# Optimization experiments

Measured on AMD Instinct MI355X. Metric: run time of the kernel, lower is better.

The kernel has to match this reference:

```python
import jax, jax.numpy as jnp
import numpy as np

N, D = 16384, 2048


def setup_inputs() -> dict:
    key = jax.random.key(0)
    k1, k2 = jax.random.split(key)
    x = jax.random.normal(k1, (N, D), dtype=jnp.float32)
    mask = jax.random.randint(k2, (N, D), 0, 2) > 0
    return {"x": x, "mask": mask}


def _masked_sparsemax(z, m):
    """Project each row of z onto the simplex restricted to positions where m is True.

    Fully batched equivalent of the TF per-row map_fn/cond/boolean_mask version.
    z: [..., D] float, m: [..., D] bool. Returns p with p>=0, sum over active = 1
    (all-zeros row if no active entries).
    """
    d = z.shape[-1]
    num_active = jnp.sum(m, axis=-1, keepdims=True)                 # [..., 1] int
    # Masked entries sort to the tail (-inf), so the first num_active sorted
    # entries are exactly the active values in descending order.
    z_neg = jnp.where(m, z, -jnp.inf)
    z_sorted = -jnp.sort(-z_neg, axis=-1)                           # descending
    k_int = jnp.arange(1, d + 1)
    k = k_int.astype(z.dtype)
    active_pos = k_int <= num_active                                # [..., D]
    # cumsum over active sorted entries only (zeros beyond num_active)
    csum = jnp.cumsum(jnp.where(active_pos, z_sorted, 0.0), axis=-1)
    # support condition: z_(k) - (csum_k - 1)/k > 0  <=>  k*z_(k) > csum_k - 1
    cond = (z_sorted * k > (csum - 1.0)) & active_pos
    rho = jnp.sum(cond, axis=-1, keepdims=True)                     # support size
    rho_idx = jnp.clip(rho - 1, 0, d - 1)
    csum_rho = jnp.take_along_axis(csum, rho_idx, axis=-1)
    theta = (csum_rho - 1.0) / jnp.maximum(rho, 1).astype(z.dtype)
    p_valid = jnp.maximum(z - theta, 0.0)
    # TF invalid_branch fallback: uniform over active entries (unreachable in
    # exact arithmetic since k=1 always satisfies cond, kept for faithfulness)
    p_uniform = 1.0 / jnp.maximum(num_active, 1).astype(z.dtype)
    p = jnp.where(rho > 0, p_valid, p_uniform)
    return jnp.where(m & (num_active > 0), p, 0.0)


def reference(x, mask):
    # axis = -1: project along the last axis (the TF layer transposes the
    # chosen axis to last; with axis=-1 that transpose is the identity).
    return _masked_sparsemax(x, mask)
```

## Files before the change

kernel.cpp:

```cpp
#include <hip/hip_runtime.h>
#include <math.h>


constexpr int D    = 2048;
constexpr int WPB  = 4;
constexpr int TPB  = WPB * 64;
constexpr int EPT  = D / 64;
constexpr int CHK  = EPT / 4;

__global__ __launch_bounds__(TPB) void sparsemax_kernel(
    const float* __restrict__ x,
    const int*   __restrict__ mask,
    float*       __restrict__ out,
    int n_rows)
{
    const int wave = threadIdx.x >> 6;
    const int lane = threadIdx.x & 63;
    const int row  = blockIdx.x * WPB + wave;
    if (row >= n_rows) return;

    const size_t rbase = (size_t)row * D;

    float z[EPT];
    #pragma unroll
    for (int c = 0; c < CHK; ++c) {
        const size_t off = rbase + (size_t)(c * 256 + lane * 4);
        const float4 a = *(const float4*)(x    + off);
        const int4   m = *(const int4*)  (mask + off);
        z[c * 4 + 0] = m.x ? a.x : -INFINITY;
        z[c * 4 + 1] = m.y ? a.y : -INFINITY;
        z[c * 4 + 2] = m.z ? a.z : -INFINITY;
        z[c * 4 + 3] = m.w ? a.w : -INFINITY;
    }

    float theta = -INFINITY;
    float prevC = -1.0f;

    for (int it = 0; it < 128; ++it) {
        float ps = 0.0f, pc = 0.0f;
        #pragma unroll
        for (int k = 0; k < EPT; ++k) {
            if (z[k] > theta) { ps += z[k]; pc += 1.0f; }
        }
        #pragma unroll
        for (int off = 32; off > 0; off >>= 1) {
            ps += __shfl_xor(ps, off, 64);
            pc += __shfl_xor(pc, off, 64);
        }
        if (pc == 0.0f) { theta = INFINITY; break; }
        if (pc == prevC) break;
        theta = (ps - 1.0f) / pc;
        prevC = pc;
    }

    #pragma unroll
    for (int c = 0; c < CHK; ++c) {
        const size_t off = rbase + (size_t)(c * 256 + lane * 4);
        float4 o;
        o.x = fmaxf(z[c * 4 + 0] - theta, 0.0f);
        o.y = fmaxf(z[c * 4 + 1] - theta, 0.0f);
        o.z = fmaxf(z[c * 4 + 2] - theta, 0.0f);
        o.w = fmaxf(z[c * 4 + 3] - theta, 0.0f);
        *(float4*)(out + off) = o;
    }
}

extern "C" void kernel_launch(void* const* d_in, const int* in_sizes, int n_in,
                              void* d_out, int out_size, void* d_ws, size_t ws_size,
                              hipStream_t stream) {
    const float* x    = (const float*)d_in[0];
    const int*   mask = (const int*)  d_in[1];
    float*       out  = (float*)d_out;
    const int n_rows = in_sizes[0] / D;
    const int blocks = (n_rows + WPB - 1) / WPB;
    sparsemax_kernel<<<blocks, TPB, 0, stream>>>(x, mask, out, n_rows);
}
```

Baseline: 313.6 us.

## Start sparsemax threshold search at max-1 and use ballot-based support counting

The threshold iteration now starts from the row maximum minus one instead of negative infinity. It updates theta with a Newton-style step based on the sum of positive excesses. The support count comes from wave ballots plus popcount instead of a per-lane float counter and shuffle reduction. The intent is fewer iterations and cheaper reductions per iteration, at the cost of an extra max reduction and one ballot per element per iteration.

Result: no change. 310.8 us (-0.9%).

```diff
diff --git a/kernel.cpp b/kernel.cpp
--- a/kernel.cpp
+++ b/kernel.cpp
@@ -33,24 +33,48 @@
         z[c * 4 + 3] = m.w ? a.w : -INFINITY;
     }
 
-    float theta = -INFINITY;
-    float prevC = -1.0f;
+    float m0 = z[0], m1 = z[1], m2 = z[2], m3 = z[3];
+    #pragma unroll
+    for (int k = 4; k < EPT; k += 4) {
+        m0 = fmaxf(m0, z[k + 0]);
+        m1 = fmaxf(m1, z[k + 1]);
+        m2 = fmaxf(m2, z[k + 2]);
+        m3 = fmaxf(m3, z[k + 3]);
+    }
+    float gmax = fmaxf(fmaxf(m0, m1), fmaxf(m2, m3));
+    #pragma unroll
+    for (int off = 32; off > 0; off >>= 1)
+        gmax = fmaxf(gmax, __shfl_xor(gmax, off, 64));
 
-    for (int it = 0; it < 128; ++it) {
-        float ps = 0.0f, pc = 0.0f;
-        #pragma unroll
-        for (int k = 0; k < EPT; ++k) {
-            if (z[k] > theta) { ps += z[k]; pc += 1.0f; }
+    float theta;
+    if (gmax == -INFINITY) {
+        theta = INFINITY;
+    } else {
+        theta = gmax - 1.0f;
+        int prevC = -1;
+        for (int it = 0; it < 64; ++it) {
+            float f0 = 0.0f, f1 = 0.0f, f2 = 0.0f, f3 = 0.0f;
+            #pragma unroll
+            for (int k = 0; k < EPT; k += 4) {
+                f0 += fmaxf(z[k + 0] - theta, 0.0f);
+                f1 += fmaxf(z[k + 1] - theta, 0.0f);
+                f2 += fmaxf(z[k + 2] - theta, 0.0f);
+                f3 += fmaxf(z[k + 3] - theta, 0.0f);
+            }
+            float f = (f0 + f1) + (f2 + f3);
+            int C = 0;
+            #pragma unroll
+            for (int k = 0; k < EPT; ++k)
+                C += (int)__popcll(__ballot(z[k] > theta));
+            #pragma unroll
+            for (int off = 32; off > 0; off >>= 1)
+                f += __shfl_xor(f, off, 64);
+
+            if (C == 0) break;
+            if (C == prevC) break;
+            theta += (f - 1.0f) / (float)C;
+            prevC = C;
         }
-        #pragma unroll
-        for (int off = 32; off > 0; off >>= 1) {
-            ps += __shfl_xor(ps, off, 64);
-            pc += __shfl_xor(pc, off, 64);
-        }
-        if (pc == 0.0f) { theta = INFINITY; break; }
-        if (pc == prevC) break;
-        theta = (ps - 1.0f) / pc;
-        prevC = pc;
     }
 
     #pragma unroll
```

## Process two rows per wave with max-initialized Newton threshold iteration

Applied to the files above, without the earlier changes.

Each wave now handles two rows, interleaving their loads and threshold iterations to raise memory-level parallelism. The threshold search starts at max-1 and takes Newton-style steps on the sum of clipped values, with the support count taken from ballot/popcount instead of per-lane float counts. Output uses nontemporal stores, and launch bounds request higher occupancy. The cost is doubled register pressure (two 32-element rows per lane), which under the occupancy hint may cause spills, and a changed convergence path that could shift floating-point results slightly.

Measured after the change: 328.9 us. 1.05x slower.

```diff
diff --git a/kernel.cpp b/kernel.cpp
--- a/kernel.cpp
+++ b/kernel.cpp
@@ -2,13 +2,15 @@
 #include <math.h>
 
 
-constexpr int D    = 2048;
-constexpr int WPB  = 4;
-constexpr int TPB  = WPB * 64;
-constexpr int EPT  = D / 64;
-constexpr int CHK  = EPT / 4;
+constexpr int D   = 2048;
+constexpr int TPB = 256;
+constexpr int EPT = D / 64;
+constexpr int CHK = EPT / 4;
+constexpr int RPB = 2 * (TPB / 64);
 
-__global__ __launch_bounds__(TPB) void sparsemax_kernel(
+typedef float nt_f4 __attribute__((ext_vector_type(4)));
+
+__global__ __launch_bounds__(TPB, 4) void sparsemax_kernel(
     const float* __restrict__ x,
     const int*   __restrict__ mask,
     float*       __restrict__ out,
@@ -16,52 +18,144 @@
 {
     const int wave = threadIdx.x >> 6;
     const int lane = threadIdx.x & 63;
-    const int row  = blockIdx.x * WPB + wave;
-    if (row >= n_rows) return;
+    const int g    = blockIdx.x * (TPB / 64) + wave;
+    const int rA   = g * 2;
+    const int rB   = rA + 1;
+    if (rA >= n_rows) return;
+    const bool hasB = (rB < n_rows);
 
-    const size_t rbase = (size_t)row * D;
+    const size_t baseA = (size_t)rA * D;
+    const size_t baseB = (size_t)rB * D;
 
-    float z[EPT];
+    float4 xa[CHK]; int4 ma[CHK];
     #pragma unroll
     for (int c = 0; c < CHK; ++c) {
-        const size_t off = rbase + (size_t)(c * 256 + lane * 4);
-        const float4 a = *(const float4*)(x    + off);
-        const int4   m = *(const int4*)  (mask + off);
-        z[c * 4 + 0] = m.x ? a.x : -INFINITY;
-        z[c * 4 + 1] = m.y ? a.y : -INFINITY;
-        z[c * 4 + 2] = m.z ? a.z : -INFINITY;
-        z[c * 4 + 3] = m.w ? a.w : -INFINITY;
+        const size_t off = baseA + (size_t)(c * 256 + lane * 4);
+        xa[c] = *(const float4*)(x    + off);
+        ma[c] = *(const int4*)  (mask + off);
+    }
+    float zA[EPT];
+    #pragma unroll
+    for (int c = 0; c < CHK; ++c) {
+        zA[c * 4 + 0] = ma[c].x ? xa[c].x : -INFINITY;
+        zA[c * 4 + 1] = ma[c].y ? xa[c].y : -INFINITY;
+        zA[c * 4 + 2] = ma[c].z ? xa[c].z : -INFINITY;
+        zA[c * 4 + 3] = ma[c].w ? xa[c].w : -INFINITY;
     }
 
-    float theta = -INFINITY;
-    float prevC = -1.0f;
+    float4 xb[CHK]; int4 mb[CHK];
+    if (hasB) {
+        #pragma unroll
+        for (int c = 0; c < CHK; ++c) {
+            const size_t off = baseB + (size_t)(c * 256 + lane * 4);
+            xb[c] = *(const float4*)(x    + off);
+            mb[c] = *(const int4*)  (mask + off);
+        }
+    }
 
-    for (int it = 0; it < 128; ++it) {
-        float ps = 0.0f, pc = 0.0f;
+    float m0 = zA[0], m1 = zA[1], m2 = zA[2], m3 = zA[3];
+    #pragma unroll
+    for (int k = 4; k < EPT; k += 4) {
+        m0 = fmaxf(m0, zA[k + 0]);
+        m1 = fmaxf(m1, zA[k + 1]);
+        m2 = fmaxf(m2, zA[k + 2]);
+        m3 = fmaxf(m3, zA[k + 3]);
+    }
+    float gmaxA = fmaxf(fmaxf(m0, m1), fmaxf(m2, m3));
+    #pragma unroll
+    for (int off = 32; off > 0; off >>= 1)
+        gmaxA = fmaxf(gmaxA, __shfl_xor(gmaxA, off, 64));
+
+    float zB[EPT];
+    if (hasB) {
+        #pragma unroll
+        for (int c = 0; c < CHK; ++c) {
+            zB[c * 4 + 0] = mb[c].x ? xb[c].x : -INFINITY;
+            zB[c * 4 + 1] = mb[c].y ? xb[c].y : -INFINITY;
+            zB[c * 4 + 2] = mb[c].z ? xb[c].z : -INFINITY;
+            zB[c * 4 + 3] = mb[c].w ? xb[c].w : -INFINITY;
+        }
+    } else {
+        #pragma unroll
+        for (int k = 0; k < EPT; ++k) zB[k] = -INFINITY;
+    }
+    m0 = zB[0]; m1 = zB[1]; m2 = zB[2]; m3 = zB[3];
+    #pragma unroll
+    for (int k = 4; k < EPT; k += 4) {
+        m0 = fmaxf(m0, zB[k + 0]);
+        m1 = fmaxf(m1, zB[k + 1]);
+        m2 = fmaxf(m2, zB[k + 2]);
+        m3 = fmaxf(m3, zB[k + 3]);
+    }
+    float gmaxB = fmaxf(fmaxf(m0, m1), fmaxf(m2, m3));
+    #pragma unroll
+    for (int off = 32; off > 0; off >>= 1)
+        gmaxB = fmaxf(gmaxB, __shfl_xor(gmaxB, off, 64));
+
+    bool doneA = (gmaxA == -INFINITY);
+    bool doneB = (gmaxB == -INFINITY);
+    float thA = doneA ? INFINITY : gmaxA - 1.0f;
+    float thB = doneB ? INFINITY : gmaxB - 1.0f;
+    int pcA = -1, pcB = -1;
+
+    for (int it = 0; it < 64 && !(doneA && doneB); ++it) {
+        float a0 = 0.f, a1 = 0.f, a2 = 0.f, a3 = 0.f;
+        float b0 = 0.f, b1 = 0.f, b2 = 0.f, b3 = 0.f;
+        #pragma unroll
+        for (int k = 0; k < EPT; k += 4) {
+            a0 += fmaxf(zA[k + 0] - thA, 0.0f);
+            a1 += fmaxf(zA[k + 1] - thA, 0.0f);
+            a2 += fmaxf(zA[k + 2] - thA, 0.0f);
+            a3 += fmaxf(zA[k + 3] - thA, 0.0f);
+            b0 += fmaxf(zB[k + 0] - thB, 0.0f);
+            b1 += fmaxf(zB[k + 1] - thB, 0.0f);
+            b2 += fmaxf(zB[k + 2] - thB, 0.0f);
+            b3 += fmaxf(zB[k + 3] - thB, 0.0f);
+        }
+        float fA = (a0 + a1) + (a2 + a3);
+        float fB = (b0 + b1) + (b2 + b3);
+        int CA = 0, CB = 0;
         #pragma unroll
         for (int k = 0; k < EPT; ++k) {
-            if (z[k] > theta) { ps += z[k]; pc += 1.0f; }
+            CA += (int)__popcll(__ballot(zA[k] > thA));
+            CB += (int)__popcll(__ballot(zB[k] > thB));
         }
         #pragma unroll
         for (int off = 32; off > 0; off >>= 1) {
-            ps += __shfl_xor(ps, off, 64);
-            pc += __shfl_xor(pc, off, 64);
+            fA += __shfl_xor(fA, off, 64);
+            fB += __shfl_xor(fB, off, 64);
         }
-        if (pc == 0.0f) { theta = INFINITY; break; }
-        if (pc == prevC) break;
-        theta = (ps - 1.0f) / pc;
-        prevC = pc;
+        if (!doneA) {
+            if (CA == 0 || CA == pcA) doneA = true;
+            else { thA += (fA - 1.0f) / (float)CA; pcA = CA; }
+        }
+        if (!doneB) {
+            if (CB == 0 || CB == pcB) doneB = true;
+            else { thB += (fB - 1.0f) / (float)CB; pcB = CB; }
+        }
     }
 
     #pragma unroll
     for (int c = 0; c < CHK; ++c) {
-        const size_t off = rbase + (size_t)(c * 256 + lane * 4);
-        float4 o;
-        o.x = fmaxf(z[c * 4 + 0] - theta, 0.0f);
-        o.y = fmaxf(z[c * 4 + 1] - theta, 0.0f);
-        o.z = fmaxf(z[c * 4 + 2] - theta, 0.0f);
-        o.w = fmaxf(z[c * 4 + 3] - theta, 0.0f);
-        *(float4*)(out + off) = o;
+        const size_t off = baseA + (size_t)(c * 256 + lane * 4);
+        nt_f4 o;
+        o.x = fmaxf(zA[c * 4 + 0] - thA, 0.0f);
+        o.y = fmaxf(zA[c * 4 + 1] - thA, 0.0f);
+        o.z = fmaxf(zA[c * 4 + 2] - thA, 0.0f);
+        o.w = fmaxf(zA[c * 4 + 3] - thA, 0.0f);
+        __builtin_nontemporal_store(o, (nt_f4*)(out + off));
+    }
+    if (hasB) {
+        #pragma unroll
+        for (int c = 0; c < CHK; ++c) {
+            const size_t off = baseB + (size_t)(c * 256 + lane * 4);
+            nt_f4 o;
+            o.x = fmaxf(zB[c * 4 + 0] - thB, 0.0f);
+            o.y = fmaxf(zB[c * 4 + 1] - thB, 0.0f);
+            o.z = fmaxf(zB[c * 4 + 2] - thB, 0.0f);
+            o.w = fmaxf(zB[c * 4 + 3] - thB, 0.0f);
+            __builtin_nontemporal_store(o, (nt_f4*)(out + off));
+        }
     }
 }
 
@@ -72,6 +166,6 @@
     const int*   mask = (const int*)  d_in[1];
     float*       out  = (float*)d_out;
     const int n_rows = in_sizes[0] / D;
-    const int blocks = (n_rows + WPB - 1) / WPB;
+    const int blocks = (n_rows + RPB - 1) / RPB;
     sparsemax_kernel<<<blocks, TPB, 0, stream>>>(x, mask, out, n_rows);
 }
```
